# Optimization experiments

Hardware: AMD Instinct MI355X
Metric: run time of the kernel (lower is better)

The kernel has to match this reference:

```python
import jax, jax.numpy as jnp
import numpy as np

N_HEADS = 8
HEAD_DIM = 64  # hidden_dim 512 / 8 heads
EPS = 1e-12    # F.normalize clamp_min eps


def setup_inputs() -> dict:
    key = jax.random.key(0)
    k1, k2, k3, k4 = jax.random.split(key, 4)
    B, C, H, W = 2, 256, 48, 48
    hidden = N_HEADS * HEAD_DIM
    x = jax.random.normal(k1, (B, C, H, W), dtype=jnp.float32)
    w_qkv = jax.random.normal(k2, (hidden * 3, C), dtype=jnp.float32) * 0.02
    w_proj = jax.random.normal(k3, (C, hidden), dtype=jnp.float32) * 0.02
    b_proj = jax.random.normal(k4, (C,), dtype=jnp.float32) * 0.02
    return {"x": x, "w_qkv": w_qkv, "w_proj": w_proj, "b_proj": b_proj}


def _l2norm_tokens(t):
    # normalize along the token axis (last dim), matching F.normalize(dim=-1)
    n = jnp.sqrt(jnp.sum(t * t, axis=-1, keepdims=True))
    return t / jnp.maximum(n, EPS)


def reference(x, w_qkv, w_proj, b_proj):
    B, C, H, W = x.shape
    N = H * W
    # 1x1 conv == channel matmul
    qkv = jnp.einsum('oc,bchw->bohw', w_qkv, x)  # [B, 3*hidden, H, W]
    qkv = qkv.reshape(B, 3, N_HEADS, HEAD_DIM, N)
    q, k, v = qkv[:, 0], qkv[:, 1], qkv[:, 2]    # each [B, h, d, N]
    q = _l2norm_tokens(q)
    k = _l2norm_tokens(k)
    # attn = q^T @ k over head_dim -> [B, h, N, N]; note: qk_scale unused in source
    attn = jnp.einsum('bhdn,bhdm->bhnm', q, k)
    attn = jax.nn.softmax(attn, axis=-1)
    # out = attn @ v^T -> [B, h, N, d], then permute to [B, h, d, N]
    out = jnp.einsum('bhnm,bhdm->bhdn', attn, v)
    out = out.reshape(B, N_HEADS * HEAD_DIM, H, W)
    # proj 1x1 conv with bias
    y = jnp.einsum('oc,bchw->bohw', w_proj, out) + b_proj[None, :, None, None]
    return y
```

## Files before the change

kernel.cpp:

```cpp
#include <hip/hip_runtime.h>
#include <math.h>

#define NTOK 2304
#define BATCH 2
#define CIN 256
#define HID 512
#define NH 8
#define LOG2E 1.44269504088896340736f

typedef __attribute__((ext_vector_type(8))) short bfrag;
typedef __attribute__((ext_vector_type(16))) float f32x16;

#if __has_builtin(__builtin_amdgcn_exp2f)
#define EXP2(x) __builtin_amdgcn_exp2f(x)
#else
#define EXP2(x) exp2f(x)
#endif

__device__ __forceinline__ unsigned f2bf(float f) {
    unsigned u = __float_as_uint(f);
    u += 0x7FFF + ((u >> 16) & 1);
    return u >> 16;
}

__device__ __forceinline__ float bf2f(unsigned short s) {
    return __uint_as_float(((unsigned)s) << 16);
}

__device__ __forceinline__ unsigned pk_trunc(float a, float b) {
    return __builtin_amdgcn_perm(__float_as_uint(b), __float_as_uint(a), 0x07060302u);
}

__device__ __forceinline__ void softmax_frag(
    const f32x16& accS, int h, float& ps0, float& ps1, bfrag& P0, bfrag& P1)
{
    unsigned dw[8];
    float e0[8], e1[8];
#pragma unroll
    for (int i = 0; i < 8; i++) {
        float plo = EXP2(accS[2 * i]);
        float phi = EXP2(accS[2 * i + 1]);
        dw[i] = pk_trunc(plo, phi);
        e0[i] = __uint_as_float(dw[i] << 16);
        e1[i] = __uint_as_float(dw[i] & 0xffff0000u);
    }
    ps0 += ((e0[0] + e0[1]) + (e0[2] + e0[3])) + ((e0[4] + e0[5]) + (e0[6] + e0[7]));
    ps1 += ((e1[0] + e1[1]) + (e1[2] + e1[3])) + ((e1[4] + e1[5]) + (e1[6] + e1[7]));
    unsigned sa0 = h ? dw[0] : dw[2], sb0 = h ? dw[1] : dw[3];
    unsigned sa1 = h ? dw[4] : dw[6], sb1 = h ? dw[5] : dw[7];
    unsigned ra0 = (unsigned)__shfl_xor((int)sa0, 32, 64);
    unsigned rb0 = (unsigned)__shfl_xor((int)sb0, 32, 64);
    unsigned ra1 = (unsigned)__shfl_xor((int)sa1, 32, 64);
    unsigned rb1 = (unsigned)__shfl_xor((int)sb1, 32, 64);
    union { bfrag f; unsigned u[4]; } U0, U1;
    U0.u[0] = h ? ra0 : dw[0];  U0.u[1] = h ? rb0 : dw[1];
    U0.u[2] = h ? dw[2] : ra0;  U0.u[3] = h ? dw[3] : rb0;
    U1.u[0] = h ? ra1 : dw[4];  U1.u[1] = h ? rb1 : dw[5];
    U1.u[2] = h ? dw[6] : ra1;  U1.u[3] = h ? dw[7] : rb1;
    P0 = U0.f; P1 = U1.f;
}

__global__ __launch_bounds__(256) void pack_all(
    const float* __restrict__ wq, short* __restrict__ wqb,
    const float* __restrict__ wp, short* __restrict__ wpb,
    const float* __restrict__ x, short* __restrict__ xT,
    float* __restrict__ sumsq)
{
    int bid = blockIdx.x;
    if (bid < 288) {
        int n0 = (bid % 36) * 64, c0 = ((bid / 36) & 3) * 64, b = bid / 144;
        __shared__ float sT[64][65];
        int tid = threadIdx.x, lane = tid & 63, wv = tid >> 6;
        for (int c = wv; c < 64; c += 4)
            sT[c][lane] = x[((size_t)b * CIN + c0 + c) * NTOK + n0 + lane];
        __syncthreads();
        int n = tid >> 2, c4 = (tid & 3) * 16;
        unsigned buf[8];
#pragma unroll
        for (int i = 0; i < 8; i++)
            buf[i] = f2bf(sT[c4 + 2 * i][n]) | (f2bf(sT[c4 + 2 * i + 1][n]) << 16);
        int n_tok = n0 + n;
        int l31n = n & 31;
        short* dst = xT + (((size_t)b * 72 + (n_tok >> 5)) * 16 + ((c0 + c4) >> 4)) * 512;
        ((uint4*)(dst + (0 * 32 + l31n) * 8))[0] = make_uint4(buf[0], buf[1], buf[2], buf[3]);
        ((uint4*)(dst + (1 * 32 + l31n) * 8))[0] = make_uint4(buf[4], buf[5], buf[6], buf[7]);
    } else {
        if (bid == 288) {
            ((float4*)sumsq)[threadIdx.x * 2] = make_float4(0.f, 0.f, 0.f, 0.f);
            ((float4*)sumsq)[threadIdx.x * 2 + 1] = make_float4(0.f, 0.f, 0.f, 0.f);
        }
        int e = ((bid - 288) * 256 + threadIdx.x) * 8;
        const int NQ = 1536 * 256;
        const float* src; short* dst;
        if (e < NQ) {
            int row = e >> 8, c = e & 255;
            int off = (((row >> 5) * 16 + (c >> 4)) * 64 + ((c >> 3) & 1) * 32 + (row & 31)) * 8;
            src = wq + e; dst = wqb + off;
        } else {
            int e2 = e - NQ;
            int row = e2 >> 9, c = e2 & 511;
            int off = (((row >> 5) * 32 + (c >> 4)) * 64 + ((c >> 3) & 1) * 32 + (row & 31)) * 8;
            src = wp + e2; dst = wpb + off;
        }
        float4 v0 = ((const float4*)src)[0];
        float4 v1 = ((const float4*)src)[1];
        unsigned b0 = f2bf(v0.x) | (f2bf(v0.y) << 16);
        unsigned b1 = f2bf(v0.z) | (f2bf(v0.w) << 16);
        unsigned b2 = f2bf(v1.x) | (f2bf(v1.y) << 16);
        unsigned b3 = f2bf(v1.z) | (f2bf(v1.w) << 16);
        *((uint4*)dst) = make_uint4(b0, b1, b2, b3);
    }
}

__global__ __launch_bounds__(256, 2) void gemm_qkv(
    const short* __restrict__ A,
    const short* __restrict__ B,
    short* __restrict__ qku,
    short* __restrict__ vb)
{
    int b = blockIdx.z;
    int o0 = blockIdx.y * 128;
    int n0 = blockIdx.x * 128;
    int tid = threadIdx.x, wv = tid >> 6, lane = tid & 63;
    int h = lane >> 5, l31 = lane & 31;

    const short* pa = A + ((size_t)(o0 >> 5) * 16) * 512 + lane * 8;
    const short* pb = B + (((size_t)b * 72 + (n0 >> 5) + wv) * 16) * 512 + lane * 8;

    f32x16 acc[4];
#pragma unroll
    for (int rb = 0; rb < 4; rb++)
#pragma unroll
        for (int r = 0; r < 16; r++) acc[rb][r] = 0.f;

#pragma unroll 2
    for (int kc = 0; kc < 16; kc++) {
        bfrag a0 = *(const bfrag*)(pa + (size_t)(0 * 16 + kc) * 512);
        bfrag a1 = *(const bfrag*)(pa + (size_t)(1 * 16 + kc) * 512);
        bfrag a2 = *(const bfrag*)(pa + (size_t)(2 * 16 + kc) * 512);
        bfrag a3 = *(const bfrag*)(pa + (size_t)(3 * 16 + kc) * 512);
        bfrag bb = *(const bfrag*)(pb + (size_t)kc * 512);
        acc[0] = __builtin_amdgcn_mfma_f32_32x32x16_bf16(a0, bb, acc[0], 0, 0, 0);
        acc[1] = __builtin_amdgcn_mfma_f32_32x32x16_bf16(a1, bb, acc[1], 0, 0, 0);
        acc[2] = __builtin_amdgcn_mfma_f32_32x32x16_bf16(a2, bb, acc[2], 0, 0, 0);
        acc[3] = __builtin_amdgcn_mfma_f32_32x32x16_bf16(a3, bb, acc[3], 0, 0, 0);
    }

    int nn = n0 + wv * 32 + l31;
    if (o0 < 1024) {
        int sel = o0 >> 9;
        short* Qb = qku + (size_t)sel * (16 * NTOK * 64);
        int oo = o0 & 511;
        int tl = nn & 31;
        size_t base_mb = (size_t)(nn >> 5) * 4;
#pragma unroll
        for (int rb = 0; rb < 4; rb++) {
            int hh2 = (oo + rb * 32) >> 6;
            int ihi = (rb & 1) * 2;
            short* Qbb = Qb + (size_t)(b * 8 + hh2) * (NTOK * 64);
#pragma unroll
            for (int q = 0; q < 4; q++) {
                int i = ihi + (q >> 1);
                unsigned lo = f2bf(acc[rb][4 * q])     | (f2bf(acc[rb][4 * q + 1]) << 16);
                unsigned hi = f2bf(acc[rb][4 * q + 2]) | (f2bf(acc[rb][4 * q + 3]) << 16);
                *(uint2*)(Qbb + (base_mb + i) * 512 + ((q & 1) * 32 + tl) * 8 + 4 * h)
                    = make_uint2(lo, hi);
            }
        }
    } else {
        short* V = vb + (size_t)b * 512 * NTOK;
        int ov = o0 - 1024;
        int mb = nn >> 5, jc = (nn >> 4) & 1, hv = (nn >> 3) & 1, e = nn & 7;
#pragma unroll
        for (int rb = 0; rb < 4; rb++)
#pragma unroll
            for (int r = 0; r < 16; r++) {
                int ml = (r & 3) + 8 * (r >> 2) + 4 * h;
                int row = ov + rb * 32 + ml;
                int hh2 = row >> 6, dl = row & 63;
                int jr = dl >> 5, l31v = dl & 31;
                V[((((size_t)hh2 * 72 + mb) * 4 + jr * 2 + jc) * 64
                   + hv * 32 + l31v) * 8 + e] = (short)f2bf(acc[rb][r]);
            }
    }
}

__global__ __launch_bounds__(64) void sumsq_qk(
    const short* __restrict__ qkt, float* __restrict__ sumsq)
{
    int bid = blockIdx.x;
    int mc = bid % 9;
    int rest = bid / 9;
    int i = rest & 3;
    int selbh = rest >> 2;
    int lane = threadIdx.x;
    const short* p = qkt + (((size_t)selbh * 72 + mc * 8) * 4 + i) * 512 + lane * 8;
    float sq[8] = {0.f, 0.f, 0.f, 0.f, 0.f, 0.f, 0.f, 0.f};
#pragma unroll
    for (int m = 0; m < 8; m++) {
        bfrag v = *(const bfrag*)(p + (size_t)m * 2048);
#pragma unroll
        for (int e = 0; e < 8; e++) {
            float f = bf2f((unsigned short)v[e]);
            sq[e] += f * f;
        }
    }
#pragma unroll
    for (int off = 1; off <= 16; off <<= 1)
#pragma unroll
        for (int e = 0; e < 8; e++)
            sq[e] += __shfl_xor(sq[e], off, 64);
    if ((lane & 31) == 0) {
        int sel = selbh >> 4, bh = selbh & 15;
        int b = bh >> 3, hh = bh & 7, hsel = lane >> 5;
        int dbase = i * 16 + hsel * 8;
        float* dst = sumsq + b * 1024 + sel * 512 + hh * 64 + dbase;
#pragma unroll
        for (int e = 0; e < 8; e++) atomicAdd(dst + e, sq[e]);
    }
}

__global__ __launch_bounds__(256) void scale_qk(
    short* __restrict__ qkt, const float* __restrict__ sumsq)
{
    int s = blockIdx.x * 256 + threadIdx.x;
    int lane = s & 63;
    int rest = s >> 6;
    int fi = rest & 3;
    int selbh = rest / 288;
    int sel = selbh >> 4, bh = selbh & 15;
    int b = bh >> 3, hh = bh & 7;
    int d0 = fi * 16 + (lane >> 5) * 8;
    const float* sp = sumsq + b * 1024 + sel * 512 + hh * 64 + d0;
    float scl = sel == 0 ? LOG2E : 1.f;
    float4 s0 = ((const float4*)sp)[0];
    float4 s1 = ((const float4*)sp)[1];
    float i0 = scl / fmaxf(sqrtf(s0.x), 1e-12f);
    float i1 = scl / fmaxf(sqrtf(s0.y), 1e-12f);
    float i2 = scl / fmaxf(sqrtf(s0.z), 1e-12f);
    float i3 = scl / fmaxf(sqrtf(s0.w), 1e-12f);
    float i4 = scl / fmaxf(sqrtf(s1.x), 1e-12f);
    float i5 = scl / fmaxf(sqrtf(s1.y), 1e-12f);
    float i6 = scl / fmaxf(sqrtf(s1.z), 1e-12f);
    float i7 = scl / fmaxf(sqrtf(s1.w), 1e-12f);
    uint4 v = ((uint4*)qkt)[s];
    unsigned o0w = f2bf(__uint_as_float(v.x << 16) * i0)
                 | (f2bf(__uint_as_float(v.x & 0xffff0000u) * i1) << 16);
    unsigned o1w = f2bf(__uint_as_float(v.y << 16) * i2)
                 | (f2bf(__uint_as_float(v.y & 0xffff0000u) * i3) << 16);
    unsigned o2w = f2bf(__uint_as_float(v.z << 16) * i4)
                 | (f2bf(__uint_as_float(v.z & 0xffff0000u) * i5) << 16);
    unsigned o3w = f2bf(__uint_as_float(v.w << 16) * i6)
                 | (f2bf(__uint_as_float(v.w & 0xffff0000u) * i7) << 16);
    ((uint4*)qkt)[s] = make_uint4(o0w, o1w, o2w, o3w);
}

__global__ __launch_bounds__(128, 2) void attn_nb(
    const short* __restrict__ qkt,
    const short* __restrict__ vb,
    short* __restrict__ Opart,
    float* __restrict__ lsum)
{
    int bid = blockIdx.x;
    int g = bid & 63;
    int bh = g >> 2, ms = g & 3;
    int ntile = bid >> 6;
    int b = bh >> 3, hh = bh & 7;
    int tid = threadIdx.x, wv = tid >> 6, lane = tid & 63;
    int h = lane >> 5, l31 = lane & 31;
    int nb0 = ntile * 128 + wv * 32;
    int nb1 = nb0 + 64;
    int mb0 = ms * 18;

    const short* Qt = qkt + (size_t)bh * NTOK * 64;
    const short* kp = qkt + (size_t)16 * NTOK * 64 + (size_t)bh * NTOK * 64
                    + ((size_t)mb0 * 4) * 512 + lane * 8;
    const short* vp = vb + (((size_t)(b * 8 + hh) * 72 + mb0) * 4) * 512 + lane * 8;

    bfrag bQ0[4], bQ1[4];
    {
        const short* q0 = Qt + ((size_t)(nb0 >> 5) * 4) * 512 + lane * 8;
        const short* q1 = Qt + ((size_t)(nb1 >> 5) * 4) * 512 + lane * 8;
#pragma unroll
        for (int i = 0; i < 4; i++) {
            bQ0[i] = *(const bfrag*)(q0 + i * 512);
            bQ1[i] = *(const bfrag*)(q1 + i * 512);
        }
    }

    f32x16 aL0, aH0, aL1, aH1;
#pragma unroll
    for (int r = 0; r < 16; r++) { aL0[r] = 0.f; aH0[r] = 0.f; aL1[r] = 0.f; aH1[r] = 0.f; }
    float s00 = 0.f, s01 = 0.f, s10 = 0.f, s11 = 0.f;

    bfrag ck[4], cv[4];
#pragma unroll
    for (int i = 0; i < 4; i++) {
        ck[i] = *(const bfrag*)(kp + i * 512);
        cv[i] = *(const bfrag*)(vp + i * 512);
    }

#pragma unroll 2
    for (int it = 0; it < 18; it++) {
        kp += 2048; vp += 2048;
        bfrag nk[4], nv[4];
#pragma unroll
        for (int i = 0; i < 4; i++) {
            nk[i] = *(const bfrag*)(kp + i * 512);
            nv[i] = *(const bfrag*)(vp + i * 512);
        }

        bfrag P00, P01, P10, P11;
        {
            f32x16 accS;
#pragma unroll
            for (int r = 0; r < 16; r++) accS[r] = 0.f;
            accS = __builtin_amdgcn_mfma_f32_32x32x16_bf16(ck[0], bQ0[0], accS, 0, 0, 0);
            accS = __builtin_amdgcn_mfma_f32_32x32x16_bf16(ck[1], bQ0[1], accS, 0, 0, 0);
            accS = __builtin_amdgcn_mfma_f32_32x32x16_bf16(ck[2], bQ0[2], accS, 0, 0, 0);
            accS = __builtin_amdgcn_mfma_f32_32x32x16_bf16(ck[3], bQ0[3], accS, 0, 0, 0);
            softmax_frag(accS, h, s00, s01, P00, P01);
        }
        {
            f32x16 accS;
#pragma unroll
            for (int r = 0; r < 16; r++) accS[r] = 0.f;
            accS = __builtin_amdgcn_mfma_f32_32x32x16_bf16(ck[0], bQ1[0], accS, 0, 0, 0);
            accS = __builtin_amdgcn_mfma_f32_32x32x16_bf16(ck[1], bQ1[1], accS, 0, 0, 0);
            accS = __builtin_amdgcn_mfma_f32_32x32x16_bf16(ck[2], bQ1[2], accS, 0, 0, 0);
            accS = __builtin_amdgcn_mfma_f32_32x32x16_bf16(ck[3], bQ1[3], accS, 0, 0, 0);
            softmax_frag(accS, h, s10, s11, P10, P11);
        }
        aL0 = __builtin_amdgcn_mfma_f32_32x32x16_bf16(P00, cv[0], aL0, 0, 0, 0);
        aL0 = __builtin_amdgcn_mfma_f32_32x32x16_bf16(P01, cv[1], aL0, 0, 0, 0);
        aH0 = __builtin_amdgcn_mfma_f32_32x32x16_bf16(P00, cv[2], aH0, 0, 0, 0);
        aH0 = __builtin_amdgcn_mfma_f32_32x32x16_bf16(P01, cv[3], aH0, 0, 0, 0);
        aL1 = __builtin_amdgcn_mfma_f32_32x32x16_bf16(P10, cv[0], aL1, 0, 0, 0);
        aL1 = __builtin_amdgcn_mfma_f32_32x32x16_bf16(P11, cv[1], aL1, 0, 0, 0);
        aH1 = __builtin_amdgcn_mfma_f32_32x32x16_bf16(P10, cv[2], aH1, 0, 0, 0);
        aH1 = __builtin_amdgcn_mfma_f32_32x32x16_bf16(P11, cv[3], aH1, 0, 0, 0);

#pragma unroll
        for (int i = 0; i < 4; i++) { ck[i] = nk[i]; cv[i] = nv[i]; }
    }

    float p0 = s00 + s01;
    p0 += __shfl_xor(p0, 32, 64);
    float p1 = s10 + s11;
    p1 += __shfl_xor(p1, 32, 64);
    if (h == 0) {
        lsum[((size_t)ms * 16 + bh) * NTOK + nb0 + l31] = p0;
        lsum[((size_t)ms * 16 + bh) * NTOK + nb1 + l31] = p1;
    }

    short* Ob = Opart + ((size_t)ms * 2 + b) * (72 * 32 * 64 * 8);
    int nbs0 = nb0 >> 5, nbs1 = nb1 >> 5;
    int kcL = hh * 4 + (l31 >> 4);
    int kcH = kcL + 2;
    int e = l31 & 7;
    int hs8 = ((l31 >> 3) & 1) * 32;
#pragma unroll
    for (int r = 0; r < 16; r++) {
        int ml = (r & 3) + 8 * (r >> 2) + 4 * h;
        int wi = hs8 + ml;
        Ob[(((size_t)nbs0 * 32 + kcL) * 64 + wi) * 8 + e] = (short)f2bf(aL0[r]);
        Ob[(((size_t)nbs0 * 32 + kcH) * 64 + wi) * 8 + e] = (short)f2bf(aH0[r]);
        Ob[(((size_t)nbs1 * 32 + kcL) * 64 + wi) * 8 + e] = (short)f2bf(aL1[r]);
        Ob[(((size_t)nbs1 * 32 + kcH) * 64 + wi) * 8 + e] = (short)f2bf(aH1[r]);
    }
}

__global__ __launch_bounds__(256) void combine(
    const short* __restrict__ Opart, const float* __restrict__ lsum,
    short* __restrict__ aoT)
{
    int s = blockIdx.x * 256 + threadIdx.x;
    int lane = s & 63, kc = (s >> 6) & 31, nbb = s >> 11;
    int b = nbb >= 72 ? 1 : 0, nb = nbb - 72 * b;
    int l31 = lane & 31;
    int n = nb * 32 + l31;
    int hh = kc >> 2;
    float l = 0.f;
#pragma unroll
    for (int ms = 0; ms < 4; ms++)
        l += lsum[((size_t)ms * 16 + b * 8 + hh) * NTOK + n];
    float inv = 1.f / l;
    const size_t MS = 2ull * 72 * 32 * 64 * 8;
    float a[8] = {0.f, 0.f, 0.f, 0.f, 0.f, 0.f, 0.f, 0.f};
#pragma unroll
    for (int ms = 0; ms < 4; ms++) {
        uint4 v = *(const uint4*)(Opart + (size_t)ms * MS + (size_t)s * 8);
        a[0] += __uint_as_float(v.x << 16);
        a[1] += __uint_as_float(v.x & 0xffff0000u);
        a[2] += __uint_as_float(v.y << 16);
        a[3] += __uint_as_float(v.y & 0xffff0000u);
        a[4] += __uint_as_float(v.z << 16);
        a[5] += __uint_as_float(v.z & 0xffff0000u);
        a[6] += __uint_as_float(v.w << 16);
        a[7] += __uint_as_float(v.w & 0xffff0000u);
    }
    unsigned b0 = f2bf(a[0] * inv) | (f2bf(a[1] * inv) << 16);
    unsigned b1 = f2bf(a[2] * inv) | (f2bf(a[3] * inv) << 16);
    unsigned b2 = f2bf(a[4] * inv) | (f2bf(a[5] * inv) << 16);
    unsigned b3 = f2bf(a[6] * inv) | (f2bf(a[7] * inv) << 16);
    *((uint4*)(aoT + (size_t)s * 8)) = make_uint4(b0, b1, b2, b3);
}

__global__ __launch_bounds__(256, 2) void gemm_proj(
    const short* __restrict__ A,
    const short* __restrict__ B,
    const float* __restrict__ bias, float* __restrict__ y)
{
    int b = blockIdx.z;
    int o0 = blockIdx.y * 64;
    int n0 = blockIdx.x * 128;
    int tid = threadIdx.x, wv = tid >> 6, lane = tid & 63;
    int h = lane >> 5, l31 = lane & 31;

    const short* pa = A + ((size_t)(o0 >> 5) * 32) * 512 + lane * 8;
    const short* pb = B + (((size_t)b * 72 + (n0 >> 5) + wv) * 32) * 512 + lane * 8;

    f32x16 acc0, acc1;
#pragma unroll
    for (int r = 0; r < 16; r++) { acc0[r] = 0.f; acc1[r] = 0.f; }

#pragma unroll 4
    for (int kc = 0; kc < 32; kc++) {
        bfrag a0 = *(const bfrag*)(pa + (size_t)kc * 512);
        bfrag a1 = *(const bfrag*)(pa + (size_t)(32 + kc) * 512);
        bfrag bb = *(const bfrag*)(pb + (size_t)kc * 512);
        acc0 = __builtin_amdgcn_mfma_f32_32x32x16_bf16(a0, bb, acc0, 0, 0, 0);
        acc1 = __builtin_amdgcn_mfma_f32_32x32x16_bf16(a1, bb, acc1, 0, 0, 0);
    }

    int nn = n0 + wv * 32 + l31;
#pragma unroll
    for (int r = 0; r < 16; r++) {
        int ml = (r & 3) + 8 * (r >> 2) + 4 * h;
        y[((size_t)b * CIN + o0 + ml) * NTOK + nn] = acc0[r] + bias[o0 + ml];
        y[((size_t)b * CIN + o0 + 32 + ml) * NTOK + nn] = acc1[r] + bias[o0 + 32 + ml];
    }
}

extern "C" void kernel_launch(void* const* d_in, const int* in_sizes, int n_in,
                              void* d_out, int out_size, void* d_ws, size_t ws_size,
                              hipStream_t stream)
{
    const float* x      = (const float*)d_in[0];
    const float* w_qkv  = (const float*)d_in[1];
    const float* w_proj = (const float*)d_in[2];
    const float* b_proj = (const float*)d_in[3];
    float* y = (float*)d_out;

    short* Opart = (short*)d_ws;
    short* vb    = (short*)((char*)d_ws + 18874368);
    short* qkt   = (short*)((char*)d_ws + 23592960);
    short* aoT   = (short*)((char*)d_ws + 23592960);
    float* lsum  = (float*)((char*)d_ws + 33030144);
    short* xT    = (short*)((char*)d_ws + 33030144);
    short* wqb   = (short*)((char*)d_ws + 35389440);
    short* wpb   = (short*)((char*)d_ws + 36175872);
    float* sumsq = (float*)((char*)d_ws + 36438016);

    pack_all<<<544, 256, 0, stream>>>(w_qkv, wqb, w_proj, wpb, x, xT, sumsq);
    gemm_qkv<<<dim3(NTOK / 128, 1536 / 128, BATCH), 256, 0, stream>>>(
        wqb, xT, qkt, vb);
    sumsq_qk<<<1152, 64, 0, stream>>>(qkt, sumsq);
    scale_qk<<<2304, 256, 0, stream>>>(qkt, sumsq);
    attn_nb<<<1152, 128, 0, stream>>>(qkt, vb, Opart, lsum);
    combine<<<1152, 256, 0, stream>>>(Opart, lsum, aoT);
    gemm_proj<<<dim3(NTOK / 128, CIN / 64, BATCH), 256, 0, stream>>>(
        wpb, aoT, b_proj, y);
}
```

Before: 143.8 us.

## Share K/V tiles via LDS across four waves and fold K norm into Q

```diff
diff --git a/kernel.cpp b/kernel.cpp
--- a/kernel.cpp
+++ b/kernel.cpp
@@ -220,29 +220,28 @@
     }
 }
 
-__global__ __launch_bounds__(256) void scale_qk(
+__global__ __launch_bounds__(256) void scale_q(
     short* __restrict__ qkt, const float* __restrict__ sumsq)
 {
     int s = blockIdx.x * 256 + threadIdx.x;
     int lane = s & 63;
     int rest = s >> 6;
     int fi = rest & 3;
-    int selbh = rest / 288;
-    int sel = selbh >> 4, bh = selbh & 15;
+    int bh = rest / 288;
     int b = bh >> 3, hh = bh & 7;
     int d0 = fi * 16 + (lane >> 5) * 8;
-    const float* sp = sumsq + b * 1024 + sel * 512 + hh * 64 + d0;
-    float scl = sel == 0 ? LOG2E : 1.f;
-    float4 s0 = ((const float4*)sp)[0];
-    float4 s1 = ((const float4*)sp)[1];
-    float i0 = scl / fmaxf(sqrtf(s0.x), 1e-12f);
-    float i1 = scl / fmaxf(sqrtf(s0.y), 1e-12f);
-    float i2 = scl / fmaxf(sqrtf(s0.z), 1e-12f);
-    float i3 = scl / fmaxf(sqrtf(s0.w), 1e-12f);
-    float i4 = scl / fmaxf(sqrtf(s1.x), 1e-12f);
-    float i5 = scl / fmaxf(sqrtf(s1.y), 1e-12f);
-    float i6 = scl / fmaxf(sqrtf(s1.z), 1e-12f);
-    float i7 = scl / fmaxf(sqrtf(s1.w), 1e-12f);
+    const float* sq = sumsq + b * 1024 + hh * 64 + d0;
+    const float* sk = sumsq + b * 1024 + 512 + hh * 64 + d0;
+    float4 q0 = ((const float4*)sq)[0], q1 = ((const float4*)sq)[1];
+    float4 k0 = ((const float4*)sk)[0], k1 = ((const float4*)sk)[1];
+    float i0 = LOG2E / (fmaxf(sqrtf(q0.x), 1e-12f) * fmaxf(sqrtf(k0.x), 1e-12f));
+    float i1 = LOG2E / (fmaxf(sqrtf(q0.y), 1e-12f) * fmaxf(sqrtf(k0.y), 1e-12f));
+    float i2 = LOG2E / (fmaxf(sqrtf(q0.z), 1e-12f) * fmaxf(sqrtf(k0.z), 1e-12f));
+    float i3 = LOG2E / (fmaxf(sqrtf(q0.w), 1e-12f) * fmaxf(sqrtf(k0.w), 1e-12f));
+    float i4 = LOG2E / (fmaxf(sqrtf(q1.x), 1e-12f) * fmaxf(sqrtf(k1.x), 1e-12f));
+    float i5 = LOG2E / (fmaxf(sqrtf(q1.y), 1e-12f) * fmaxf(sqrtf(k1.y), 1e-12f));
+    float i6 = LOG2E / (fmaxf(sqrtf(q1.z), 1e-12f) * fmaxf(sqrtf(k1.z), 1e-12f));
+    float i7 = LOG2E / (fmaxf(sqrtf(q1.w), 1e-12f) * fmaxf(sqrtf(k1.w), 1e-12f));
     uint4 v = ((uint4*)qkt)[s];
     unsigned o0w = f2bf(__uint_as_float(v.x << 16) * i0)
                  | (f2bf(__uint_as_float(v.x & 0xffff0000u) * i1) << 16);
@@ -255,7 +254,7 @@
     ((uint4*)qkt)[s] = make_uint4(o0w, o1w, o2w, o3w);
 }
 
-__global__ __launch_bounds__(128, 2) void attn_nb(
+__global__ __launch_bounds__(256, 2) void attn_nb(
     const short* __restrict__ qkt,
     const short* __restrict__ vb,
     short* __restrict__ Opart,
@@ -268,14 +267,18 @@
     int b = bh >> 3, hh = bh & 7;
     int tid = threadIdx.x, wv = tid >> 6, lane = tid & 63;
     int h = lane >> 5, l31 = lane & 31;
-    int nb0 = ntile * 128 + wv * 32;
-    int nb1 = nb0 + 64;
+    int nb0 = ntile * 256 + wv * 32;
+    int nb1 = nb0 + 128;
     int mb0 = ms * 18;
+
+    __shared__ short kls[2][2048];
+    __shared__ short vls[2][2048];
 
     const short* Qt = qkt + (size_t)bh * NTOK * 64;
     const short* kp = qkt + (size_t)16 * NTOK * 64 + (size_t)bh * NTOK * 64
-                    + ((size_t)mb0 * 4) * 512 + lane * 8;
-    const short* vp = vb + (((size_t)(b * 8 + hh) * 72 + mb0) * 4) * 512 + lane * 8;
+                    + ((size_t)mb0 * 4) * 512 + wv * 512 + lane * 8;
+    const short* vp = vb + (((size_t)(b * 8 + hh) * 72 + mb0) * 4) * 512
+                    + wv * 512 + lane * 8;
 
     bfrag bQ0[4], bQ1[4];
     {
@@ -293,21 +296,29 @@
     for (int r = 0; r < 16; r++) { aL0[r] = 0.f; aH0[r] = 0.f; aL1[r] = 0.f; aH1[r] = 0.f; }
     float s00 = 0.f, s01 = 0.f, s10 = 0.f, s11 = 0.f;
 
-    bfrag ck[4], cv[4];
-#pragma unroll
-    for (int i = 0; i < 4; i++) {
-        ck[i] = *(const bfrag*)(kp + i * 512);
-        cv[i] = *(const bfrag*)(vp + i * 512);
-    }
-
+    {
+        bfrag k0 = *(const bfrag*)kp;
+        bfrag v0 = *(const bfrag*)vp;
+        *(bfrag*)&kls[0][wv * 512 + lane * 8] = k0;
+        *(bfrag*)&vls[0][wv * 512 + lane * 8] = v0;
+    }
+    __syncthreads();
+
+    int cur = 0;
 #pragma unroll 2
     for (int it = 0; it < 18; it++) {
-        kp += 2048; vp += 2048;
-        bfrag nk[4], nv[4];
+        bfrag nk, nv;
+        if (it < 17) {
+            kp += 2048; vp += 2048;
+            nk = *(const bfrag*)kp;
+            nv = *(const bfrag*)vp;
+        }
+
+        bfrag ck[4], cv[4];
 #pragma unroll
         for (int i = 0; i < 4; i++) {
-            nk[i] = *(const bfrag*)(kp + i * 512);
-            nv[i] = *(const bfrag*)(vp + i * 512);
+            ck[i] = *(const bfrag*)&kls[cur][i * 512 + lane * 8];
+            cv[i] = *(const bfrag*)&vls[cur][i * 512 + lane * 8];
         }
 
         bfrag P00, P01, P10, P11;
@@ -340,8 +351,12 @@
         aH1 = __builtin_amdgcn_mfma_f32_32x32x16_bf16(P10, cv[2], aH1, 0, 0, 0);
         aH1 = __builtin_amdgcn_mfma_f32_32x32x16_bf16(P11, cv[3], aH1, 0, 0, 0);
 
-#pragma unroll
-        for (int i = 0; i < 4; i++) { ck[i] = nk[i]; cv[i] = nv[i]; }
+        if (it < 17) {
+            *(bfrag*)&kls[cur ^ 1][wv * 512 + lane * 8] = nk;
+            *(bfrag*)&vls[cur ^ 1][wv * 512 + lane * 8] = nv;
+        }
+        __syncthreads();
+        cur ^= 1;
     }
 
     float p0 = s00 + s01;
@@ -466,8 +481,8 @@
     gemm_qkv<<<dim3(NTOK / 128, 1536 / 128, BATCH), 256, 0, stream>>>(
         wqb, xT, qkt, vb);
     sumsq_qk<<<1152, 64, 0, stream>>>(qkt, sumsq);
-    scale_qk<<<2304, 256, 0, stream>>>(qkt, sumsq);
-    attn_nb<<<1152, 128, 0, stream>>>(qkt, vb, Opart, lsum);
+    scale_q<<<1152, 256, 0, stream>>>(qkt, sumsq);
+    attn_nb<<<576, 256, 0, stream>>>(qkt, vb, Opart, lsum);
     combine<<<1152, 256, 0, stream>>>(Opart, lsum, aoT);
     gemm_proj<<<dim3(NTOK / 128, CIN / 64, BATCH), 256, 0, stream>>>(
         wpb, aoT, b_proj, y);
```

Result: no change. 144.9 us (+0.8%).

## Fold K normalization into Q scaling and split attention into single-wave blocks

Applied to the files above, without the earlier changes.

```diff
diff --git a/kernel.cpp b/kernel.cpp
--- a/kernel.cpp
+++ b/kernel.cpp
@@ -220,29 +220,28 @@
     }
 }
 
-__global__ __launch_bounds__(256) void scale_qk(
+__global__ __launch_bounds__(256) void scale_q(
     short* __restrict__ qkt, const float* __restrict__ sumsq)
 {
     int s = blockIdx.x * 256 + threadIdx.x;
     int lane = s & 63;
     int rest = s >> 6;
     int fi = rest & 3;
-    int selbh = rest / 288;
-    int sel = selbh >> 4, bh = selbh & 15;
+    int bh = rest / 288;
     int b = bh >> 3, hh = bh & 7;
     int d0 = fi * 16 + (lane >> 5) * 8;
-    const float* sp = sumsq + b * 1024 + sel * 512 + hh * 64 + d0;
-    float scl = sel == 0 ? LOG2E : 1.f;
-    float4 s0 = ((const float4*)sp)[0];
-    float4 s1 = ((const float4*)sp)[1];
-    float i0 = scl / fmaxf(sqrtf(s0.x), 1e-12f);
-    float i1 = scl / fmaxf(sqrtf(s0.y), 1e-12f);
-    float i2 = scl / fmaxf(sqrtf(s0.z), 1e-12f);
-    float i3 = scl / fmaxf(sqrtf(s0.w), 1e-12f);
-    float i4 = scl / fmaxf(sqrtf(s1.x), 1e-12f);
-    float i5 = scl / fmaxf(sqrtf(s1.y), 1e-12f);
-    float i6 = scl / fmaxf(sqrtf(s1.z), 1e-12f);
-    float i7 = scl / fmaxf(sqrtf(s1.w), 1e-12f);
+    const float* sq = sumsq + b * 1024 + hh * 64 + d0;
+    const float* sk = sumsq + b * 1024 + 512 + hh * 64 + d0;
+    float4 q0 = ((const float4*)sq)[0], q1 = ((const float4*)sq)[1];
+    float4 k0 = ((const float4*)sk)[0], k1 = ((const float4*)sk)[1];
+    float i0 = LOG2E / (fmaxf(sqrtf(q0.x), 1e-12f) * fmaxf(sqrtf(k0.x), 1e-12f));
+    float i1 = LOG2E / (fmaxf(sqrtf(q0.y), 1e-12f) * fmaxf(sqrtf(k0.y), 1e-12f));
+    float i2 = LOG2E / (fmaxf(sqrtf(q0.z), 1e-12f) * fmaxf(sqrtf(k0.z), 1e-12f));
+    float i3 = LOG2E / (fmaxf(sqrtf(q0.w), 1e-12f) * fmaxf(sqrtf(k0.w), 1e-12f));
+    float i4 = LOG2E / (fmaxf(sqrtf(q1.x), 1e-12f) * fmaxf(sqrtf(k1.x), 1e-12f));
+    float i5 = LOG2E / (fmaxf(sqrtf(q1.y), 1e-12f) * fmaxf(sqrtf(k1.y), 1e-12f));
+    float i6 = LOG2E / (fmaxf(sqrtf(q1.z), 1e-12f) * fmaxf(sqrtf(k1.z), 1e-12f));
+    float i7 = LOG2E / (fmaxf(sqrtf(q1.w), 1e-12f) * fmaxf(sqrtf(k1.w), 1e-12f));
     uint4 v = ((uint4*)qkt)[s];
     unsigned o0w = f2bf(__uint_as_float(v.x << 16) * i0)
                  | (f2bf(__uint_as_float(v.x & 0xffff0000u) * i1) << 16);
@@ -255,21 +254,22 @@
     ((uint4*)qkt)[s] = make_uint4(o0w, o1w, o2w, o3w);
 }
 
-__global__ __launch_bounds__(128, 2) void attn_nb(
+__global__ __launch_bounds__(64, 4) void attn_nb(
     const short* __restrict__ qkt,
     const short* __restrict__ vb,
     short* __restrict__ Opart,
     float* __restrict__ lsum)
 {
     int bid = blockIdx.x;
-    int g = bid & 63;
+    int x = bid & 7;
+    int r = bid >> 3;
+    int g = x * 8 + r / 72;
+    int nbi = r % 72;
     int bh = g >> 2, ms = g & 3;
-    int ntile = bid >> 6;
     int b = bh >> 3, hh = bh & 7;
-    int tid = threadIdx.x, wv = tid >> 6, lane = tid & 63;
+    int lane = threadIdx.x;
     int h = lane >> 5, l31 = lane & 31;
-    int nb0 = ntile * 128 + wv * 32;
-    int nb1 = nb0 + 64;
+    int nb = nbi * 32;
     int mb0 = ms * 18;
 
     const short* Qt = qkt + (size_t)bh * NTOK * 64;
@@ -277,21 +277,17 @@
                     + ((size_t)mb0 * 4) * 512 + lane * 8;
     const short* vp = vb + (((size_t)(b * 8 + hh) * 72 + mb0) * 4) * 512 + lane * 8;
 
-    bfrag bQ0[4], bQ1[4];
+    bfrag bQ[4];
     {
-        const short* q0 = Qt + ((size_t)(nb0 >> 5) * 4) * 512 + lane * 8;
-        const short* q1 = Qt + ((size_t)(nb1 >> 5) * 4) * 512 + lane * 8;
-#pragma unroll
-        for (int i = 0; i < 4; i++) {
-            bQ0[i] = *(const bfrag*)(q0 + i * 512);
-            bQ1[i] = *(const bfrag*)(q1 + i * 512);
-        }
-    }
-
-    f32x16 aL0, aH0, aL1, aH1;
-#pragma unroll
-    for (int r = 0; r < 16; r++) { aL0[r] = 0.f; aH0[r] = 0.f; aL1[r] = 0.f; aH1[r] = 0.f; }
-    float s00 = 0.f, s01 = 0.f, s10 = 0.f, s11 = 0.f;
+        const short* q0 = Qt + ((size_t)nbi * 4) * 512 + lane * 8;
+#pragma unroll
+        for (int i = 0; i < 4; i++) bQ[i] = *(const bfrag*)(q0 + i * 512);
+    }
+
+    f32x16 aL, aH;
+#pragma unroll
+    for (int r2 = 0; r2 < 16; r2++) { aL[r2] = 0.f; aH[r2] = 0.f; }
+    float s0 = 0.f, s1 = 0.f;
 
     bfrag ck[4], cv[4];
 #pragma unroll
@@ -310,63 +306,42 @@
             nv[i] = *(const bfrag*)(vp + i * 512);
         }
 
-        bfrag P00, P01, P10, P11;
+        bfrag P0, P1;
         {
             f32x16 accS;
 #pragma unroll
-            for (int r = 0; r < 16; r++) accS[r] = 0.f;
-            accS = __builtin_amdgcn_mfma_f32_32x32x16_bf16(ck[0], bQ0[0], accS, 0, 0, 0);
-            accS = __builtin_amdgcn_mfma_f32_32x32x16_bf16(ck[1], bQ0[1], accS, 0, 0, 0);
-            accS = __builtin_amdgcn_mfma_f32_32x32x16_bf16(ck[2], bQ0[2], accS, 0, 0, 0);
-            accS = __builtin_amdgcn_mfma_f32_32x32x16_bf16(ck[3], bQ0[3], accS, 0, 0, 0);
-            softmax_frag(accS, h, s00, s01, P00, P01);
-        }
-        {
-            f32x16 accS;
-#pragma unroll
-            for (int r = 0; r < 16; r++) accS[r] = 0.f;
-            accS = __builtin_amdgcn_mfma_f32_32x32x16_bf16(ck[0], bQ1[0], accS, 0, 0, 0);
-            accS = __builtin_amdgcn_mfma_f32_32x32x16_bf16(ck[1], bQ1[1], accS, 0, 0, 0);
-            accS = __builtin_amdgcn_mfma_f32_32x32x16_bf16(ck[2], bQ1[2], accS, 0, 0, 0);
-            accS = __builtin_amdgcn_mfma_f32_32x32x16_bf16(ck[3], bQ1[3], accS, 0, 0, 0);
-            softmax_frag(accS, h, s10, s11, P10, P11);
-        }
-        aL0 = __builtin_amdgcn_mfma_f32_32x32x16_bf16(P00, cv[0], aL0, 0, 0, 0);
-        aL0 = __builtin_amdgcn_mfma_f32_32x32x16_bf16(P01, cv[1], aL0, 0, 0, 0);
-        aH0 = __builtin_amdgcn_mfma_f32_32x32x16_bf16(P00, cv[2], aH0, 0, 0, 0);
-        aH0 = __builtin_amdgcn_mfma_f32_32x32x16_bf16(P01, cv[3], aH0, 0, 0, 0);
-        aL1 = __builtin_amdgcn_mfma_f32_32x32x16_bf16(P10, cv[0], aL1, 0, 0, 0);
-        aL1 = __builtin_amdgcn_mfma_f32_32x32x16_bf16(P11, cv[1], aL1, 0, 0, 0);
-        aH1 = __builtin_amdgcn_mfma_f32_32x32x16_bf16(P10, cv[2], aH1, 0, 0, 0);
-        aH1 = __builtin_amdgcn_mfma_f32_32x32x16_bf16(P11, cv[3], aH1, 0, 0, 0);
+            for (int r2 = 0; r2 < 16; r2++) accS[r2] = 0.f;
+            accS = __builtin_amdgcn_mfma_f32_32x32x16_bf16(ck[0], bQ[0], accS, 0, 0, 0);
+            accS = __builtin_amdgcn_mfma_f32_32x32x16_bf16(ck[1], bQ[1], accS, 0, 0, 0);
+            accS = __builtin_amdgcn_mfma_f32_32x32x16_bf16(ck[2], bQ[2], accS, 0, 0, 0);
+            accS = __builtin_amdgcn_mfma_f32_32x32x16_bf16(ck[3], bQ[3], accS, 0, 0, 0);
+            softmax_frag(accS, h, s0, s1, P0, P1);
+        }
+        aL = __builtin_amdgcn_mfma_f32_32x32x16_bf16(P0, cv[0], aL, 0, 0, 0);
+        aL = __builtin_amdgcn_mfma_f32_32x32x16_bf16(P1, cv[1], aL, 0, 0, 0);
+        aH = __builtin_amdgcn_mfma_f32_32x32x16_bf16(P0, cv[2], aH, 0, 0, 0);
+        aH = __builtin_amdgcn_mfma_f32_32x32x16_bf16(P1, cv[3], aH, 0, 0, 0);
 
 #pragma unroll
         for (int i = 0; i < 4; i++) { ck[i] = nk[i]; cv[i] = nv[i]; }
     }
 
-    float p0 = s00 + s01;
+    float p0 = s0 + s1;
     p0 += __shfl_xor(p0, 32, 64);
-    float p1 = s10 + s11;
-    p1 += __shfl_xor(p1, 32, 64);
-    if (h == 0) {
-        lsum[((size_t)ms * 16 + bh) * NTOK + nb0 + l31] = p0;
-        lsum[((size_t)ms * 16 + bh) * NTOK + nb1 + l31] = p1;
-    }
+    if (h == 0)
+        lsum[((size_t)ms * 16 + bh) * NTOK + nb + l31] = p0;
 
     short* Ob = Opart + ((size_t)ms * 2 + b) * (72 * 32 * 64 * 8);
-    int nbs0 = nb0 >> 5, nbs1 = nb1 >> 5;
     int kcL = hh * 4 + (l31 >> 4);
     int kcH = kcL + 2;
     int e = l31 & 7;
     int hs8 = ((l31 >> 3) & 1) * 32;
 #pragma unroll
-    for (int r = 0; r < 16; r++) {
-        int ml = (r & 3) + 8 * (r >> 2) + 4 * h;
+    for (int r2 = 0; r2 < 16; r2++) {
+        int ml = (r2 & 3) + 8 * (r2 >> 2) + 4 * h;
         int wi = hs8 + ml;
-        Ob[(((size_t)nbs0 * 32 + kcL) * 64 + wi) * 8 + e] = (short)f2bf(aL0[r]);
-        Ob[(((size_t)nbs0 * 32 + kcH) * 64 + wi) * 8 + e] = (short)f2bf(aH0[r]);
-        Ob[(((size_t)nbs1 * 32 + kcL) * 64 + wi) * 8 + e] = (short)f2bf(aL1[r]);
-        Ob[(((size_t)nbs1 * 32 + kcH) * 64 + wi) * 8 + e] = (short)f2bf(aH1[r]);
+        Ob[(((size_t)nbi * 32 + kcL) * 64 + wi) * 8 + e] = (short)f2bf(aL[r2]);
+        Ob[(((size_t)nbi * 32 + kcH) * 64 + wi) * 8 + e] = (short)f2bf(aH[r2]);
     }
 }
 
@@ -466,8 +441,8 @@
     gemm_qkv<<<dim3(NTOK / 128, 1536 / 128, BATCH), 256, 0, stream>>>(
         wqb, xT, qkt, vb);
     sumsq_qk<<<1152, 64, 0, stream>>>(qkt, sumsq);
-    scale_qk<<<2304, 256, 0, stream>>>(qkt, sumsq);
-    attn_nb<<<1152, 128, 0, stream>>>(qkt, vb, Opart, lsum);
+    scale_q<<<1152, 256, 0, stream>>>(qkt, sumsq);
+    attn_nb<<<4608, 64, 0, stream>>>(qkt, vb, Opart, lsum);
     combine<<<1152, 256, 0, stream>>>(Opart, lsum, aoT);
     gemm_proj<<<dim3(NTOK / 128, CIN / 64, BATCH), 256, 0, stream>>>(
         wpb, aoT, b_proj, y);
```

After: 141.9 us. About the same (-1.3%).
